# Kernel optimization log

Measured on AMD Instinct MI355X. Metric: run time of the kernel, lower is better.

Reference implementation:

```python
import jax, jax.numpy as jnp
import numpy as np

DIM = 1024
EPS = 1e-5


def setup_inputs() -> dict:
    key = jax.random.key(0)
    ks = jax.random.split(key, 7)
    C = DIM
    x = jax.random.normal(ks[0], (4, 4096, C), dtype=jnp.float32)
    norm_w = jnp.ones((C,), dtype=jnp.float32)
    norm_b = jnp.zeros((C,), dtype=jnp.float32)
    s = 1.0 / np.sqrt(C)
    qkv_w = jax.random.uniform(ks[1], (3 * C, C), dtype=jnp.float32, minval=-s, maxval=s)
    qkv_b = jax.random.uniform(ks[2], (3 * C,), dtype=jnp.float32, minval=-s, maxval=s)
    proj_w = jax.random.uniform(ks[3], (C, C), dtype=jnp.float32, minval=-s, maxval=s)
    proj_b = jax.random.uniform(ks[4], (C,), dtype=jnp.float32, minval=-s, maxval=s)
    return {"x": x, "norm_w": norm_w, "norm_b": norm_b, "qkv_w": qkv_w,
            "qkv_b": qkv_b, "proj_w": proj_w, "proj_b": proj_b}


def _layernorm(x, w, b):
    mu = jnp.mean(x, axis=-1, keepdims=True)
    var = jnp.mean(jnp.square(x - mu), axis=-1, keepdims=True)
    return (x - mu) * jax.lax.rsqrt(var + EPS) * w + b


def reference(x, norm_w, norm_b, qkv_w, qkv_b, proj_w, proj_b):
    B, T, C = x.shape
    residual = x
    h = _layernorm(x, norm_w, norm_b)
    qkv = jnp.einsum('btc,oc->bto', h, qkv_w) + qkv_b  # [B,T,3C]
    q, k, v = qkv[..., :C], qkv[..., C:2 * C], qkv[..., 2 * C:]
    attn = jnp.einsum('btc,bsc->bts', q, k) / jnp.sqrt(jnp.float32(C))  # raw QK^T, no softmax
    o = jnp.einsum('bts,bsc->btc', attn, v)
    o = jnp.einsum('btc,oc->bto', o, proj_w) + proj_b
    return residual + o  # dropout is identity in eval mode
```

## Files before the change

kernel.cpp:

```cpp
#include <hip/hip_runtime.h>

typedef _Float16 f16;
typedef _Float16 f16x4 __attribute__((ext_vector_type(4)));
typedef _Float16 f16x8 __attribute__((ext_vector_type(8)));
typedef float f32x4 __attribute__((ext_vector_type(4)));

#define AS1 __attribute__((address_space(1)))
#define AS3 __attribute__((address_space(3)))

__device__ __forceinline__ void gl_lds16(const f16* g, f16* l) {
  __builtin_amdgcn_global_load_lds((const AS1 void*)g, (AS3 void*)l, 16, 0, 0);
}

__global__ __launch_bounds__(256) void ln_kernel(const float* __restrict__ x,
                                                 const float* __restrict__ gw,
                                                 const float* __restrict__ gb,
                                                 f16* __restrict__ H) {
  const int wv = threadIdx.x >> 6, lane = threadIdx.x & 63;
  const long row = (long)blockIdx.x * 4 + wv;
  const float* xr = x + row * 1024;
  float4 v[4];
  float s = 0.f, s2 = 0.f;
#pragma unroll
  for (int j = 0; j < 4; ++j) {
    v[j] = ((const float4*)xr)[lane + 64 * j];
    s  += v[j].x + v[j].y + v[j].z + v[j].w;
    s2 += v[j].x * v[j].x + v[j].y * v[j].y + v[j].z * v[j].z + v[j].w * v[j].w;
  }
#pragma unroll
  for (int off = 32; off > 0; off >>= 1) {
    s  += __shfl_xor(s, off);
    s2 += __shfl_xor(s2, off);
  }
  const float mu = s * (1.0f / 1024.0f);
  const float rstd = rsqrtf(s2 * (1.0f / 1024.0f) - mu * mu + 1e-5f);
#pragma unroll
  for (int j = 0; j < 4; ++j) {
    const float4 w4 = ((const float4*)gw)[lane + 64 * j];
    const float4 b4 = ((const float4*)gb)[lane + 64 * j];
    f16x4 h;
    h[0] = (f16)((v[j].x - mu) * rstd * w4.x + b4.x);
    h[1] = (f16)((v[j].y - mu) * rstd * w4.y + b4.y);
    h[2] = (f16)((v[j].z - mu) * rstd * w4.z + b4.z);
    h[3] = (f16)((v[j].w - mu) * rstd * w4.w + b4.w);
    *(f16x4*)(H + row * 1024 + (lane + 64 * j) * 4) = h;
  }
}

__global__ __launch_bounds__(256) void transpose_cs_kernel(const f16* __restrict__ H,
                                                           f16* __restrict__ Ht,
                                                           float* __restrict__ hs) {
  __shared__ f16 tile[64][68];
  __shared__ float csum[4][64];
  const int b = blockIdx.z;
  const long Hb  = (long)b * 4096 * 1024;
  const long Htb = (long)b * 1024 * 4096;
  const int t0 = blockIdx.y * 64, c0 = blockIdx.x * 64;
  const int tid = threadIdx.x;
  const int r = tid >> 2, g0 = tid & 3;
#pragma unroll
  for (int i = 0; i < 4; ++i) {
    const int g = g0 + i * 4;
    f16x4 v = *(const f16x4*)(H + Hb + (long)(t0 + r) * 1024 + c0 + g * 4);
    *(f16x4*)&tile[r][g * 4] = v;
  }
  __syncthreads();
  {
    const int cl = tid & 63, rg = tid >> 6;
    float s = 0.f;
#pragma unroll
    for (int rr = 0; rr < 16; ++rr) s += (float)tile[rg * 16 + rr][cl];
    csum[rg][cl] = s;
  }
#pragma unroll
  for (int i = 0; i < 4; ++i) {
    const int g = g0 + i * 4;
    f16x4 v;
    v[0] = tile[g * 4 + 0][r];
    v[1] = tile[g * 4 + 1][r];
    v[2] = tile[g * 4 + 2][r];
    v[3] = tile[g * 4 + 3][r];
    *(f16x4*)(Ht + Htb + (long)(c0 + r) * 4096 + t0 + g * 4) = v;
  }
  __syncthreads();
  if (tid < 64)
    atomicAdd(&hs[b * 1024 + c0 + tid],
              csum[0][tid] + csum[1][tid] + csum[2][tid] + csum[3][tid]);
}

__global__ __launch_bounds__(256) void transcast4(const float* __restrict__ qkv_w,
                                                  const float* __restrict__ proj_w,
                                                  f16* __restrict__ WT3,
                                                  f16* __restrict__ Wh,
                                                  f16* __restrict__ Ph) {
  const int z = blockIdx.z;
  __shared__ f16 tile[64][68];
  const int r0 = blockIdx.y * 64, c0 = blockIdx.x * 64;
  const int tid = threadIdx.x;
  const int r = tid >> 2, g0 = tid & 3;
  if (z == 3) {
#pragma unroll
    for (int i = 0; i < 4; ++i) {
      const int g = g0 + i * 4;
      float4 v = *(const float4*)(proj_w + (long)(r0 + r) * 1024 + c0 + g * 4);
      f16x4 h; h[0]=(f16)v.x; h[1]=(f16)v.y; h[2]=(f16)v.z; h[3]=(f16)v.w;
      *(f16x4*)(Ph + (long)(r0 + r) * 1024 + c0 + g * 4) = h;
    }
    return;
  }
  const float* W = qkv_w + (long)z * 1048576;
  f16* WT = WT3 + (long)z * 1048576;
#pragma unroll
  for (int i = 0; i < 4; ++i) {
    const int g = g0 + i * 4;
    float4 v = *(const float4*)(W + (long)(r0 + r) * 1024 + c0 + g * 4);
    f16x4 h; h[0]=(f16)v.x; h[1]=(f16)v.y; h[2]=(f16)v.z; h[3]=(f16)v.w;
    *(f16x4*)&tile[r][g * 4] = h;
    if (z >= 1)
      *(f16x4*)(Wh + (long)z * 1048576 + (long)(r0 + r) * 1024 + c0 + g * 4) = h;
  }
  __syncthreads();
#pragma unroll
  for (int i = 0; i < 4; ++i) {
    const int g = g0 + i * 4;
    f16x4 v;
    v[0] = tile[g * 4 + 0][r];
    v[1] = tile[g * 4 + 1][r];
    v[2] = tile[g * 4 + 2][r];
    v[3] = tile[g * 4 + 3][r];
    *(f16x4*)(WT + (long)(c0 + r) * 1024 + r0 + g * 4) = v;
  }
}

__device__ __forceinline__ float dot1024(const f16* __restrict__ row,
                                         const float* __restrict__ v) {
  const int lane = threadIdx.x & 63;
  float s = 0.f;
#pragma unroll
  for (int j = 0; j < 2; ++j) {
    const int d = (lane + 64 * j) * 8;
    f16x8 a = *(const f16x8*)(row + d);
    float4 h0 = *(const float4*)(v + d);
    float4 h1 = *(const float4*)(v + d + 4);
    s += (float)a[0] * h0.x + (float)a[1] * h0.y + (float)a[2] * h0.z + (float)a[3] * h0.w
       + (float)a[4] * h1.x + (float)a[5] * h1.y + (float)a[6] * h1.z + (float)a[7] * h1.w;
  }
#pragma unroll
  for (int off = 32; off > 0; off >>= 1) s += __shfl_down(s, off);
  return s;
}

__device__ __forceinline__ float dotf1024(const float* __restrict__ a,
                                          const float* __restrict__ v) {
  const int lane = threadIdx.x & 63;
  float s = 0.f;
#pragma unroll
  for (int j = 0; j < 4; ++j) {
    const int d = (lane + 64 * j) * 4;
    float4 x = *(const float4*)(a + d);
    float4 q = *(const float4*)(v + d);
    s += x.x * q.x + x.y * q.y + x.z * q.z + x.w * q.w;
  }
#pragma unroll
  for (int off = 32; off > 0; off >>= 1) s += __shfl_down(s, off);
  return s;
}

__global__ void gemv3a(const f16* __restrict__ WT3, const f16* __restrict__ Ph,
                       const float* __restrict__ qkv_b, float* __restrict__ ayd,
                       float* __restrict__ scal) {
  if (blockIdx.x == 3072) {
    float s = dotf1024(qkv_b + 1024, qkv_b);
    if ((threadIdx.x & 63) == 0) scal[4] = s;
    return;
  }
  const int which = blockIdx.x >> 10, m = blockIdx.x & 1023;
  const f16* row;
  const float* v;
  if (which == 0)      { row = WT3 + (long)m * 1024;            v = qkv_b + 1024; }
  else if (which == 1) { row = WT3 + 1048576 + (long)m * 1024;  v = qkv_b; }
  else                 { row = Ph + (long)m * 1024;             v = qkv_b + 2048; }
  float s = dot1024(row, v);
  if ((threadIdx.x & 63) == 0) ayd[which * 1024 + m] = s;
}

__global__ void gemv3b(const f16* __restrict__ U, const f16* __restrict__ PWv,
                       const f16* __restrict__ Gh, const float* __restrict__ hs,
                       const float* __restrict__ ayd, float* __restrict__ efz,
                       float* __restrict__ scal) {
  if (blockIdx.x >= 12288) {
    const int b = blockIdx.x - 12288;
    float s = dotf1024(hs + b * 1024, ayd + 1024);
    if ((threadIdx.x & 63) == 0) scal[b] = s;
    return;
  }
  const int sel = blockIdx.x >> 12, r = blockIdx.x & 4095;
  const int b = r >> 10, m = r & 1023;
  const f16* row;
  const float* v;
  if (sel == 0)      { row = U + (long)m * 1024;                       v = hs + b * 1024; }
  else if (sel == 1) { row = PWv + (long)m * 1024;                     v = hs + b * 1024; }
  else               { row = Gh + (long)b * 1048576 + (long)m * 1024;  v = ayd + 1024; }
  float s = dot1024(row, v);
  if ((threadIdx.x & 63) == 0) efz[sel * 4096 + r] = s;
}

__global__ void gemvC2n(const f16* __restrict__ PWv, const float* __restrict__ efz,
                        const float* __restrict__ ayd, const float* __restrict__ scal,
                        const float* __restrict__ proj_b, float* __restrict__ c2) {
  const int b = blockIdx.x >> 10, c = blockIdx.x & 1023;
  float s = dot1024(PWv + (long)c * 1024, efz + 8192 + b * 1024);
  if ((threadIdx.x & 63) == 0) {
    const float d = ayd[2048 + c];
    c2[b * 1024 + c] = (s + d * scal[b] + scal[4] * (efz[4096 + b * 1024 + c] + 4096.f * d))
                         * 0.03125f + proj_b[c];
  }
}

#define GP64_COMMON()                                        \
  const int tid = threadIdx.x;                               \
  const int wave = tid >> 6, lane = tid & 63;                \
  const int lr = lane & 15, lk = lane >> 4;                  \
  const int srow = tid >> 3;                                 \
  const int slc  = (tid & 7) ^ (srow & 7);                   \
  const int kc0 = ((lk) ^ (lr & 7)) * 8;                     \
  const int kc1 = ((4 + lk) ^ (lr & 7)) * 8;

#define GEMM_WAIT8(NBUF_, r_)                                               \
  do {                                                                      \
    if constexpr (NBUF_ == 3) {                                             \
      if ((r_) >= 2)      asm volatile("s_waitcnt vmcnt(16)" ::: "memory"); \
      else if ((r_) == 1) asm volatile("s_waitcnt vmcnt(8)" ::: "memory");  \
      else                asm volatile("s_waitcnt vmcnt(0)" ::: "memory");  \
    } else {                                                                \
      if ((r_) >= 1)      asm volatile("s_waitcnt vmcnt(8)" ::: "memory");  \
      else                asm volatile("s_waitcnt vmcnt(0)" ::: "memory");  \
    }                                                                       \
  } while (0)

#define COMP64_HALF(asb_, bsb_, kc_)                                             \
  do {                                                                           \
    const f16* asb = (asb_);                                                     \
    const f16* bsb = (bsb_);                                                     \
    f16x8 af[4], bf[4];                                                          \
    _Pragma("unroll")                                                            \
    for (int mi = 0; mi < 4; ++mi)                                               \
      af[mi] = *(const f16x8*)(asb + (wm * 64 + mi * 16 + lr) * 64 + (kc_));     \
    _Pragma("unroll")                                                            \
    for (int ni = 0; ni < 4; ++ni)                                               \
      bf[ni] = *(const f16x8*)(bsb + (wn * 64 + ni * 16 + lr) * 64 + (kc_));     \
    _Pragma("unroll")                                                            \
    for (int mi = 0; mi < 4; ++mi)                                               \
      _Pragma("unroll")                                                          \
      for (int ni = 0; ni < 4; ++ni)                                             \
        acc[mi][ni] = __builtin_amdgcn_mfma_f32_16x16x32_f16(af[mi], bf[ni],     \
                                                             acc[mi][ni], 0, 0, 0); \
  } while (0)

#define GEMM_BODY_LOOP(NBUF_, NT_, STAGEM)                       \
  do {                                                           \
    if constexpr (NBUF_ == 3) {                                  \
      STAGEM(0, 0); STAGEM(1, 1);                                \
      int cur = 0, stg = 2;                                      \
      for (int t = 0; t < (NT_); ++t) {                          \
        if (t + 2 < (NT_)) STAGEM(stg, t + 2);                   \
        GEMM_WAIT8(3, (NT_) - 1 - t);                            \
        asm volatile("s_barrier" ::: "memory");                  \
        __builtin_amdgcn_s_setprio(1);                           \
        COMP64_HALF(&As[cur][0], &Bs[cur][0], kc0);              \
        COMP64_HALF(&As[cur][0], &Bs[cur][0], kc1);              \
        __builtin_amdgcn_s_setprio(0);                           \
        asm volatile("s_waitcnt lgkmcnt(0)" ::: "memory");       \
        asm volatile("s_barrier" ::: "memory");                  \
        cur = (cur + 1 == 3) ? 0 : cur + 1;                      \
        stg = (stg + 1 == 3) ? 0 : stg + 1;                      \
      }                                                          \
    } else {                                                     \
      STAGEM(0, 0);                                              \
      int cur = 0;                                               \
      for (int t = 0; t < (NT_); ++t) {                          \
        if (t + 1 < (NT_)) STAGEM(cur ^ 1, t + 1);               \
        GEMM_WAIT8(2, (NT_) - 1 - t);                            \
        asm volatile("s_barrier" ::: "memory");                  \
        __builtin_amdgcn_s_setprio(1);                           \
        COMP64_HALF(&As[cur][0], &Bs[cur][0], kc0);              \
        COMP64_HALF(&As[cur][0], &Bs[cur][0], kc1);              \
        __builtin_amdgcn_s_setprio(0);                           \
        asm volatile("s_waitcnt lgkmcnt(0)" ::: "memory");       \
        asm volatile("s_barrier" ::: "memory");                  \
        cur ^= 1;                                                \
      }                                                          \
    }                                                            \
  } while (0)

template <int MODE>
__global__ __launch_bounds__(256) void gemm128(
    const f16* __restrict__ A, const f16* __restrict__ B, int K,
    long sA, long sB, long sC,
    f16* __restrict__ Ch,
    const float* __restrict__ dvec, const float* __restrict__ evec,
    const float* __restrict__ fvec, const float* __restrict__ avec) {
  const int b = blockIdx.z;
  A += (long)b * sA;
  B += (long)b * sB;
  const int nx = blockIdx.y & 7;
  const int ny = blockIdx.x;

  GP64_COMMON();
  const int wm = wave >> 1, wn = wave & 1;

  __shared__ __align__(16) f16 As[3][8192];
  __shared__ __align__(16) f16 Bs[3][8192];

  const long aoffs = (long)(ny * 128 + srow) * K + slc * 8;
  const long boffs = (long)(nx * 128 + srow) * K + slc * 8;

  f32x4 zero = {0.f, 0.f, 0.f, 0.f};
  f32x4 acc[4][4];
#pragma unroll
  for (int mi = 0; mi < 4; ++mi)
#pragma unroll
    for (int ni = 0; ni < 4; ++ni) acc[mi][ni] = zero;

#define STAGE(buf, kt)                                                              \
  do {                                                                              \
    f16* asb = &As[buf][0];                                                         \
    f16* bsb = &Bs[buf][0];                                                         \
    _Pragma("unroll")                                                               \
    for (int q = 0; q < 4; ++q) {                                                   \
      gl_lds16(A + aoffs + (long)q * 32 * K + (kt) * 64, asb + q * 2048 + tid * 8); \
      gl_lds16(B + boffs + (long)q * 32 * K + (kt) * 64, bsb + q * 2048 + tid * 8); \
    }                                                                               \
  } while (0)

  const int nt = K >> 6;
  GEMM_BODY_LOOP(3, nt, STAGE);
#undef STAGE

  const long cb = (long)b * sC;
  const int m0 = ny * 128 + wm * 64;
  const int n0 = nx * 128 + wn * 64;
#pragma unroll
  for (int mi = 0; mi < 4; ++mi)
#pragma unroll
    for (int ni = 0; ni < 4; ++ni)
#pragma unroll
      for (int j = 0; j < 4; ++j) {
        const int gm = m0 + mi * 16 + lk * 4 + j;
        const int gn = n0 + ni * 16 + lr;
        float val = acc[mi][ni][j];
        if constexpr (MODE == 0) {
          Ch[cb + (long)gm * 1024 + gn] = (f16)val;
        } else {
          const float dm = dvec[gm];
          const float fm = fvec[b * 1024 + gm];
          const float en = evec[b * 1024 + gn];
          const float an = avec[gn];
          val = (val + dm * en + (fm + 4096.f * dm) * an) * 0.03125f;
          Ch[cb + (long)gm * 1024 + gn] = (f16)val;
        }
      }
}

__global__ __launch_bounds__(256) void gemmGUV(const f16* __restrict__ Ht,
                                               const f16* __restrict__ WT3,
                                               const f16* __restrict__ Ph,
                                               f16* __restrict__ part,
                                               f16* __restrict__ U,
                                               f16* __restrict__ PWv) {
  GP64_COMMON();
  const int wm = wave >> 1, wn = wave & 1;

  __shared__ __align__(16) f16 As[2][8192];
  __shared__ __align__(16) f16 Bs[2][8192];

  const int bid = blockIdx.x;
  const f16 *Ab, *Bb;
  long rs;
  int tileid = 0, zz = 0, selt = 0;
  if (bid < 576) {
    zz = bid & 15;
    tileid = bid >> 4;
    const int b = zz & 3, ks4 = zz >> 2;
    int ti = 0, trem = tileid;
    while (trem >= 8 - ti) { trem -= 8 - ti; ++ti; }
    const int tj = ti + trem;
    const f16* Hb = Ht + (long)b * 4194304;
    rs = 4096;
    Ab = Hb + (long)(ti * 128 + srow) * 4096 + (long)ks4 * 1024 + slc * 8;
    Bb = Hb + (long)(tj * 128 + srow) * 4096 + (long)ks4 * 1024 + slc * 8;
  } else {
    const int u = bid - 576;
    selt = (u >> 6) + 1;
    const int t = u & 63;
    const int ny = t >> 3, nxx = t & 7;
    const f16* A0 = (selt == 2) ? Ph : WT3;
    const f16* B0 = (selt == 2) ? (WT3 + 2097152) : (WT3 + 1048576);
    rs = 1024;
    Ab = A0 + (long)(ny * 128 + srow) * 1024 + slc * 8;
    Bb = B0 + (long)(nxx * 128 + srow) * 1024 + slc * 8;
  }

  f32x4 zero = {0.f, 0.f, 0.f, 0.f};
  f32x4 acc[4][4];
#pragma unroll
  for (int mi = 0; mi < 4; ++mi)
#pragma unroll
    for (int ni = 0; ni < 4; ++ni) acc[mi][ni] = zero;

#define STAGE(buf, kt)                                                            \
  do {                                                                            \
    f16* asb = &As[buf][0];                                                       \
    f16* bsb = &Bs[buf][0];                                                       \
    _Pragma("unroll")                                                             \
    for (int q = 0; q < 4; ++q) {                                                 \
      gl_lds16(Ab + (long)q * 32 * rs + (kt) * 64, asb + q * 2048 + tid * 8);     \
      gl_lds16(Bb + (long)q * 32 * rs + (kt) * 64, bsb + q * 2048 + tid * 8);     \
    }                                                                             \
  } while (0)

  GEMM_BODY_LOOP(2, 16, STAGE);
#undef STAGE

  if (selt == 0) {
    f16* P = part + ((long)zz * 36 + tileid) * 16384;
#pragma unroll
    for (int mi = 0; mi < 4; ++mi)
#pragma unroll
      for (int ni = 0; ni < 4; ++ni)
#pragma unroll
        for (int j = 0; j < 4; ++j) {
          const int gm = wm * 64 + mi * 16 + lk * 4 + j;
          const int gn = wn * 64 + ni * 16 + lr;
          P[gm * 128 + gn] = (f16)acc[mi][ni][j];
        }
  } else {
    const int u = bid - 576;
    const int t = u & 63;
    const int ny = t >> 3, nxx = t & 7;
    f16* C = (selt == 2) ? PWv : U;
    const int m0 = ny * 128 + wm * 64;
    const int n0 = nxx * 128 + wn * 64;
#pragma unroll
    for (int mi = 0; mi < 4; ++mi)
#pragma unroll
      for (int ni = 0; ni < 4; ++ni)
#pragma unroll
        for (int j = 0; j < 4; ++j) {
          const int gm = m0 + mi * 16 + lk * 4 + j;
          const int gn = n0 + ni * 16 + lr;
          C[(long)gm * 1024 + gn] = (f16)acc[mi][ni][j];
        }
  }
}

__global__ __launch_bounds__(512) void gemm256f(
    const f16* __restrict__ A,
    const f16* __restrict__ Bw,
    const float* __restrict__ resid,
    const float* __restrict__ c2v,
    float* __restrict__ outF) {
  const int lin = blockIdx.y * 4 + blockIdx.x;
  const int xcd = lin & 7, slot = lin >> 3;
  const int ny = xcd * 8 + (slot >> 2);
  const int nx = slot & 3;
  const int bb = ny >> 4;

  GP64_COMMON();
  const int wm = wave >> 2, wn = wave & 3;

  __shared__ __align__(16) f16 As[2][16384];
  __shared__ __align__(16) f16 Bs[2][16384];

  const f16* Ab = A + (long)ny * 262144;
  const f16* Bb = Bw + (long)bb * 1048576 + (long)nx * 262144;
  const long offs = (long)srow * 1024 + slc * 8;

  f32x4 zero = {0.f, 0.f, 0.f, 0.f};
  f32x4 acc[8][4];
#pragma unroll
  for (int mi = 0; mi < 8; ++mi)
#pragma unroll
    for (int ni = 0; ni < 4; ++ni) acc[mi][ni] = zero;

#define SA(buf, kt, q) gl_lds16(Ab + offs + (long)(q) * 65536 + (kt) * 64, &As[buf][(q) * 4096] + tid * 8)
#define SB(buf, kt, q) gl_lds16(Bb + offs + (long)(q) * 65536 + (kt) * 64, &Bs[buf][(q) * 4096] + tid * 8)

#define RD_BF(dst, bsb, kc)                                                       \
  _Pragma("unroll")                                                               \
  for (int ni = 0; ni < 4; ++ni)                                                  \
    dst[ni] = *(const f16x8*)((bsb) + (wn * 64 + ni * 16 + lr) * 64 + (kc));
#define RD_AF(dst, asb, mh, kc)                                                   \
  _Pragma("unroll")                                                               \
  for (int mi = 0; mi < 4; ++mi)                                                  \
    dst[mi] = *(const f16x8*)((asb) + (wm * 128 + (mh) * 64 + mi * 16 + lr) * 64 + (kc));
#define MF16(af_, bf_, mo)                                                        \
  __builtin_amdgcn_s_setprio(1);                                                  \
  _Pragma("unroll")                                                               \
  for (int mi = 0; mi < 4; ++mi)                                                  \
    _Pragma("unroll")                                                             \
    for (int ni = 0; ni < 4; ++ni)                                                \
      acc[(mo) + mi][ni] = __builtin_amdgcn_mfma_f32_16x16x32_f16(af_[mi], bf_[ni], \
                                                                  acc[(mo) + mi][ni], 0, 0, 0); \
  __builtin_amdgcn_s_setprio(0);

  const int nt = 16;
  SB(0, 0, 0); SB(0, 0, 1); SB(0, 0, 2); SB(0, 0, 3);
  SA(0, 0, 0); SA(0, 0, 2); SA(0, 0, 1); SA(0, 0, 3);

  int cur = 0;
  for (int t = 0; t < nt; ++t) {
    const f16* asb = &As[cur][0];
    const f16* bsb = &Bs[cur][0];
    const int nb = cur ^ 1;
    const bool st = (t + 1 < nt);
    f16x8 bf[4], af[4];

    asm volatile("s_waitcnt vmcnt(2)" ::: "memory");
    asm volatile("s_barrier" ::: "memory");
    RD_BF(bf, bsb, kc0);
    RD_AF(af, asb, 0, kc0);
    if (st) { SB(nb, t + 1, 0); SB(nb, t + 1, 1); }
    asm volatile("s_waitcnt lgkmcnt(0)" ::: "memory");
    MF16(af, bf, 0);
    asm volatile("s_barrier" ::: "memory");

    if (st) asm volatile("s_waitcnt vmcnt(2)" ::: "memory");
    else    asm volatile("s_waitcnt vmcnt(0)" ::: "memory");
    asm volatile("s_barrier" ::: "memory");
    RD_AF(af, asb, 1, kc0);
    if (st) { SB(nb, t + 1, 2); SB(nb, t + 1, 3); }
    asm volatile("s_waitcnt lgkmcnt(0)" ::: "memory");
    MF16(af, bf, 4);
    asm volatile("s_barrier" ::: "memory");

    RD_BF(bf, bsb, kc1);
    RD_AF(af, asb, 0, kc1);
    if (st) { SA(nb, t + 1, 0); SA(nb, t + 1, 2); }
    asm volatile("s_waitcnt lgkmcnt(0)" ::: "memory");
    MF16(af, bf, 0);
    asm volatile("s_barrier" ::: "memory");

    RD_AF(af, asb, 1, kc1);
    if (st) { SA(nb, t + 1, 1); SA(nb, t + 1, 3); }
    asm volatile("s_waitcnt lgkmcnt(0)" ::: "memory");
    MF16(af, bf, 4);
    asm volatile("s_barrier" ::: "memory");

    cur ^= 1;
  }
#undef SA
#undef SB
#undef RD_BF
#undef RD_AF
#undef MF16

  asm volatile("s_waitcnt vmcnt(0)" ::: "memory");
  asm volatile("s_barrier" ::: "memory");

  float* weps = ((float*)&As[0][0]) + wave * 1088;
  const int m0 = ny * 256 + wm * 128;
  const int n0 = nx * 256 + wn * 64;
  const int err = lane >> 3;
  const int ecc = (lane & 7) * 4;
  float4 cc2[2];
#pragma unroll
  for (int q = 0; q < 2; ++q)
    cc2[q] = *(const float4*)&c2v[bb * 1024 + n0 + ecc + 32 * q];

#pragma unroll
  for (int mi = 0; mi < 8; ++mi) {
#pragma unroll
    for (int ni = 0; ni < 4; ++ni)
#pragma unroll
      for (int j = 0; j < 4; ++j)
        weps[(lk * 4 + j) * 68 + ni * 16 + lr] = acc[mi][ni][j];
    asm volatile("s_waitcnt lgkmcnt(0)" ::: "memory");
#pragma unroll
    for (int h = 0; h < 2; ++h)
#pragma unroll
      for (int q = 0; q < 2; ++q) {
        const int rr = err + 8 * h;
        const int cc = ecc + 32 * q;
        float4 o = *(const float4*)&weps[rr * 68 + cc];
        const long gbase = (long)(m0 + mi * 16 + rr) * 1024 + n0 + cc;
        const float4 rv = *(const float4*)&resid[gbase];
        float4 ov;
        ov.x = o.x + rv.x + cc2[q].x;
        ov.y = o.y + rv.y + cc2[q].y;
        ov.z = o.z + rv.z + cc2[q].z;
        ov.w = o.w + rv.w + cc2[q].w;
        *(float4*)&outF[gbase] = ov;
      }
  }
}

__global__ __launch_bounds__(256) void treduce(const f16* __restrict__ part,
                                               f16* __restrict__ Gh) {
  const int tileid = blockIdx.x, b = blockIdx.y;
  int ti = 0, trem = tileid;
  while (trem >= 8 - ti) { trem -= 8 - ti; ++ti; }
  const int tj = ti + trem;
  __shared__ f16 tl[128][132];
  const int tid = threadIdx.x;
  f16* Gb = Gh + (long)b * 1048576;
#pragma unroll
  for (int it = 0; it < 16; ++it) {
    const int e = it * 1024 + tid * 4;
    const int r = e >> 7, c = e & 127;
    f16x4 p0 = *(const f16x4*)(part + ((long)(0 * 4 + b) * 36 + tileid) * 16384 + e);
    f16x4 p1 = *(const f16x4*)(part + ((long)(1 * 4 + b) * 36 + tileid) * 16384 + e);
    f16x4 p2 = *(const f16x4*)(part + ((long)(2 * 4 + b) * 36 + tileid) * 16384 + e);
    f16x4 p3 = *(const f16x4*)(part + ((long)(3 * 4 + b) * 36 + tileid) * 16384 + e);
    f16x4 sv;
#pragma unroll
    for (int j = 0; j < 4; ++j)
      sv[j] = (f16)((float)p0[j] + (float)p1[j] + (float)p2[j] + (float)p3[j]);
    *(f16x4*)(Gb + (long)(ti * 128 + r) * 1024 + tj * 128 + c) = sv;
    *(f16x4*)&tl[r][c] = sv;
  }
  if (ti != tj) {
    __syncthreads();
#pragma unroll
    for (int it = 0; it < 16; ++it) {
      const int e = it * 1024 + tid * 4;
      const int r = e >> 7, c = e & 127;
      f16x4 v;
      v[0] = tl[c + 0][r];
      v[1] = tl[c + 1][r];
      v[2] = tl[c + 2][r];
      v[3] = tl[c + 3][r];
      *(f16x4*)(Gb + (long)(tj * 128 + r) * 1024 + ti * 128 + c) = v;
    }
  }
}

extern "C" void kernel_launch(void* const* d_in, const int* in_sizes, int n_in,
                              void* d_out, int out_size, void* d_ws, size_t ws_size,
                              hipStream_t stream) {
  const float* x      = (const float*)d_in[0];
  const float* norm_w = (const float*)d_in[1];
  const float* norm_b = (const float*)d_in[2];
  const float* qkv_w  = (const float*)d_in[3];
  const float* qkv_b  = (const float*)d_in[4];
  const float* proj_w = (const float*)d_in[5];
  const float* proj_b = (const float*)d_in[6];
  float* out = (float*)d_out;
  char* ws = (char*)d_ws;

  const size_t OFF_H    = 0;
  const size_t OFF_HT   = 33554432;
  const size_t OFF_T1   = 33554432;
  const size_t OFF_T2   = 41943040;
  const size_t OFF_WH   = 67108864;
  const size_t OFF_PH   = 73400320;
  const size_t OFF_WT3  = 75497472;
  const size_t OFF_U    = 81788928;
  const size_t OFF_PWV  = 83886080;
  const size_t OFF_GH   = 85983232;
  const size_t OFF_PART = 94371840;
  const size_t OFF_HS   = 115343360;
  const size_t OFF_AYD  = 115392512;
  const size_t OFF_SCAL = 115404800;
  const size_t OFF_EFZ  = 115405824;
  const size_t OFF_C2   = 115471360;

  f16* H    = (f16*)(ws + OFF_H);
  f16* Ht   = (f16*)(ws + OFF_HT);
  f16* T1   = (f16*)(ws + OFF_T1);
  f16* T2   = (f16*)(ws + OFF_T2);
  f16* Wh   = (f16*)(ws + OFF_WH);
  f16* Ph   = (f16*)(ws + OFF_PH);
  f16* WT3  = (f16*)(ws + OFF_WT3);
  f16* U    = (f16*)(ws + OFF_U);
  f16* PWv  = (f16*)(ws + OFF_PWV);
  f16* Gh   = (f16*)(ws + OFF_GH);
  f16* part = (f16*)(ws + OFF_PART);
  float* hs   = (float*)(ws + OFF_HS);
  float* ayd  = (float*)(ws + OFF_AYD);
  float* scal = (float*)(ws + OFF_SCAL);
  float* efz  = (float*)(ws + OFF_EFZ);
  float* c2v  = (float*)(ws + OFF_C2);

  transcast4<<<dim3(16, 16, 4), 256, 0, stream>>>(qkv_w, proj_w, WT3, Wh, Ph);
  gemv3a<<<dim3(3073), 64, 0, stream>>>(WT3, Ph, qkv_b, ayd, scal);

  ln_kernel<<<dim3(4096), 256, 0, stream>>>(x, norm_w, norm_b, H);
  hipMemsetAsync(ws + OFF_HS, 0, 16384, stream);
  transpose_cs_kernel<<<dim3(16, 64, 4), 256, 0, stream>>>(H, Ht, hs);

  gemmGUV<<<dim3(704), 256, 0, stream>>>(Ht, WT3, Ph, part, U, PWv);
  treduce<<<dim3(36, 4), 256, 0, stream>>>(part, Gh);

  gemv3b<<<dim3(12292), 64, 0, stream>>>(U, PWv, Gh, hs, ayd, efz, scal);
  gemvC2n<<<dim3(4096), 64, 0, stream>>>(PWv, efz, ayd, scal, proj_b, c2v);

  gemm128<0><<<dim3(8, 8, 4), 256, 0, stream>>>(U, Gh, 1024, 0L, 1048576L, 1048576L,
      T1, nullptr, nullptr, nullptr, nullptr);
  gemm128<1><<<dim3(8, 8, 4), 256, 0, stream>>>(PWv, T1, 1024, 0L, 1048576L, 1048576L,
      T2, ayd + 2048, efz, efz + 4096, ayd);

  gemm256f<<<dim3(4, 64), 512, 0, stream>>>(H, T2, x, c2v, out);
}
```

Baseline: 195.8 us.

## Hand-schedule GEMM main loop with split A-tile prefetch and waitcnt control

Replaces the generic GEMM_BODY_LOOP in the fused GEMM kernel with a hand-written double-buffered loop. Each k-step is split into two halves, and the next tile's global-to-LDS loads are interleaved between them using explicit vmcnt/lgkmcnt waits and barriers. MFMA blocks are wrapped in s_setprio raises. The goal is to overlap memory loads with MFMA work more finely, at the cost of extra barriers and a fragile dependence on vmcnt counts matching the issue order.

```diff
diff --git a/kernel.cpp b/kernel.cpp
--- a/kernel.cpp
+++ b/kernel.cpp
@@ -408,19 +408,74 @@
 #pragma unroll
     for (int ni = 0; ni < 4; ++ni) acc[mi][ni] = zero;
 
-#define STAGE(buf, kt)                                                            \
-  do {                                                                            \
-    f16* asb = &As[buf][0];                                                       \
-    f16* bsb = &Bs[buf][0];                                                       \
-    _Pragma("unroll")                                                             \
-    for (int q = 0; q < 4; ++q) {                                                 \
-      gl_lds16(Ab + (long)q * 32 * rs + (kt) * 64, asb + q * 2048 + tid * 8);     \
-      gl_lds16(Bb + (long)q * 32 * rs + (kt) * 64, bsb + q * 2048 + tid * 8);     \
-    }                                                                             \
-  } while (0)
-
-  GEMM_BODY_LOOP(2, 16, STAGE);
-#undef STAGE
+#define SAq(buf, kt, q) gl_lds16(Ab + (long)(q) * 32 * rs + (kt) * 64, &As[buf][(q) * 2048] + tid * 8)
+#define SBq(buf, kt, q) gl_lds16(Bb + (long)(q) * 32 * rs + (kt) * 64, &Bs[buf][(q) * 2048] + tid * 8)
+
+  const int nt = 16;
+  SBq(0, 0, 0); SBq(0, 0, 1); SBq(0, 0, 2); SBq(0, 0, 3);
+  SAq(0, 0, 0); SAq(0, 0, 2); SAq(0, 0, 1); SAq(0, 0, 3);
+
+  int cur = 0;
+  for (int t = 0; t < nt; ++t) {
+    const f16* asb = &As[cur][0];
+    const f16* bsb = &Bs[cur][0];
+    const int nb = cur ^ 1;
+    const bool st = (t + 1 < nt);
+    f16x8 bf[4][2], af[2][2];
+
+    asm volatile("s_waitcnt vmcnt(2)" ::: "memory");
+    asm volatile("s_barrier" ::: "memory");
+#pragma unroll
+    for (int ni = 0; ni < 4; ++ni) {
+      bf[ni][0] = *(const f16x8*)(bsb + (wn * 64 + ni * 16 + lr) * 64 + kc0);
+      bf[ni][1] = *(const f16x8*)(bsb + (wn * 64 + ni * 16 + lr) * 64 + kc1);
+    }
+#pragma unroll
+    for (int mi = 0; mi < 2; ++mi) {
+      af[mi][0] = *(const f16x8*)(asb + (wm * 64 + mi * 16 + lr) * 64 + kc0);
+      af[mi][1] = *(const f16x8*)(asb + (wm * 64 + mi * 16 + lr) * 64 + kc1);
+    }
+    if (st) { SBq(nb, t + 1, 0); SBq(nb, t + 1, 1); SBq(nb, t + 1, 2); SBq(nb, t + 1, 3);
+              SAq(nb, t + 1, 0); SAq(nb, t + 1, 2); }
+    asm volatile("s_waitcnt lgkmcnt(0)" ::: "memory");
+    __builtin_amdgcn_s_setprio(1);
+#pragma unroll
+    for (int ks = 0; ks < 2; ++ks)
+#pragma unroll
+      for (int mi = 0; mi < 2; ++mi)
+#pragma unroll
+        for (int ni = 0; ni < 4; ++ni)
+          acc[mi][ni] = __builtin_amdgcn_mfma_f32_16x16x32_f16(af[mi][ks], bf[ni][ks],
+                                                               acc[mi][ni], 0, 0, 0);
+    __builtin_amdgcn_s_setprio(0);
+    asm volatile("s_barrier" ::: "memory");
+
+    if (st) asm volatile("s_waitcnt vmcnt(6)" ::: "memory");
+    else    asm volatile("s_waitcnt vmcnt(0)" ::: "memory");
+    asm volatile("s_barrier" ::: "memory");
+#pragma unroll
+    for (int mi = 0; mi < 2; ++mi) {
+      af[mi][0] = *(const f16x8*)(asb + (wm * 64 + (mi + 2) * 16 + lr) * 64 + kc0);
+      af[mi][1] = *(const f16x8*)(asb + (wm * 64 + (mi + 2) * 16 + lr) * 64 + kc1);
+    }
+    if (st) { SAq(nb, t + 1, 1); SAq(nb, t + 1, 3); }
+    asm volatile("s_waitcnt lgkmcnt(0)" ::: "memory");
+    __builtin_amdgcn_s_setprio(1);
+#pragma unroll
+    for (int ks = 0; ks < 2; ++ks)
+#pragma unroll
+      for (int mi = 0; mi < 2; ++mi)
+#pragma unroll
+        for (int ni = 0; ni < 4; ++ni)
+          acc[mi + 2][ni] = __builtin_amdgcn_mfma_f32_16x16x32_f16(af[mi][ks], bf[ni][ks],
+                                                                   acc[mi + 2][ni], 0, 0, 0);
+    __builtin_amdgcn_s_setprio(0);
+    asm volatile("s_barrier" ::: "memory");
+
+    cur ^= 1;
+  }
+#undef SAq
+#undef SBq
 
   if (selt == 0) {
     f16* P = part + ((long)zz * 36 + tileid) * 16384;
```

Measured after the change: 190.0 us. 2.9% less time.

## Fuse GEMV passes into batched GEMMs and use finer-grained pipelined main loop

Applied to the files above, without the earlier changes.

The standalone gemv3b and gemvC2n launches are merged into the two batched T1/T2 GEMM launches as extra blocks, with four waves per block each doing one dot product. The hs memset moves into the layernorm kernel. All three GEMMs switch to a new double-buffered loop that issues next-tile loads in quarters, interleaved between two half-tile MFMA phases. This cuts launch count and aims to overlap GEMV work with GEMM tiles, at the cost of more barriers and more complex wait counts.

```diff
diff --git a/kernel.cpp b/kernel.cpp
--- a/kernel.cpp
+++ b/kernel.cpp
@@ -15,7 +15,13 @@
 __global__ __launch_bounds__(256) void ln_kernel(const float* __restrict__ x,
                                                  const float* __restrict__ gw,
                                                  const float* __restrict__ gb,
-                                                 f16* __restrict__ H) {
+                                                 f16* __restrict__ H,
+                                                 float* __restrict__ hs) {
+  if (blockIdx.x == 0) {
+#pragma unroll
+    for (int j = 0; j < 4; ++j)
+      ((float4*)hs)[threadIdx.x + 256 * j] = make_float4(0.f, 0.f, 0.f, 0.f);
+  }
   const int wv = threadIdx.x >> 6, lane = threadIdx.x & 63;
   const long row = (long)blockIdx.x * 4 + wv;
   const float* xr = x + row * 1024;
@@ -184,39 +190,6 @@
   if ((threadIdx.x & 63) == 0) ayd[which * 1024 + m] = s;
 }
 
-__global__ void gemv3b(const f16* __restrict__ U, const f16* __restrict__ PWv,
-                       const f16* __restrict__ Gh, const float* __restrict__ hs,
-                       const float* __restrict__ ayd, float* __restrict__ efz,
-                       float* __restrict__ scal) {
-  if (blockIdx.x >= 12288) {
-    const int b = blockIdx.x - 12288;
-    float s = dotf1024(hs + b * 1024, ayd + 1024);
-    if ((threadIdx.x & 63) == 0) scal[b] = s;
-    return;
-  }
-  const int sel = blockIdx.x >> 12, r = blockIdx.x & 4095;
-  const int b = r >> 10, m = r & 1023;
-  const f16* row;
-  const float* v;
-  if (sel == 0)      { row = U + (long)m * 1024;                       v = hs + b * 1024; }
-  else if (sel == 1) { row = PWv + (long)m * 1024;                     v = hs + b * 1024; }
-  else               { row = Gh + (long)b * 1048576 + (long)m * 1024;  v = ayd + 1024; }
-  float s = dot1024(row, v);
-  if ((threadIdx.x & 63) == 0) efz[sel * 4096 + r] = s;
-}
-
-__global__ void gemvC2n(const f16* __restrict__ PWv, const float* __restrict__ efz,
-                        const float* __restrict__ ayd, const float* __restrict__ scal,
-                        const float* __restrict__ proj_b, float* __restrict__ c2) {
-  const int b = blockIdx.x >> 10, c = blockIdx.x & 1023;
-  float s = dot1024(PWv + (long)c * 1024, efz + 8192 + b * 1024);
-  if ((threadIdx.x & 63) == 0) {
-    const float d = ayd[2048 + c];
-    c2[b * 1024 + c] = (s + d * scal[b] + scal[4] * (efz[4096 + b * 1024 + c] + 4096.f * d))
-                         * 0.03125f + proj_b[c];
-  }
-}
-
 #define GP64_COMMON()                                        \
   const int tid = threadIdx.x;                               \
   const int wave = tid >> 6, lane = tid & 63;                \
@@ -226,94 +199,100 @@
   const int kc0 = ((lk) ^ (lr & 7)) * 8;                     \
   const int kc1 = ((4 + lk) ^ (lr & 7)) * 8;
 
-#define GEMM_WAIT8(NBUF_, r_)                                               \
-  do {                                                                      \
-    if constexpr (NBUF_ == 3) {                                             \
-      if ((r_) >= 2)      asm volatile("s_waitcnt vmcnt(16)" ::: "memory"); \
-      else if ((r_) == 1) asm volatile("s_waitcnt vmcnt(8)" ::: "memory");  \
-      else                asm volatile("s_waitcnt vmcnt(0)" ::: "memory");  \
-    } else {                                                                \
-      if ((r_) >= 1)      asm volatile("s_waitcnt vmcnt(8)" ::: "memory");  \
-      else                asm volatile("s_waitcnt vmcnt(0)" ::: "memory");  \
-    }                                                                       \
-  } while (0)
-
-#define COMP64_HALF(asb_, bsb_, kc_)                                             \
-  do {                                                                           \
-    const f16* asb = (asb_);                                                     \
-    const f16* bsb = (bsb_);                                                     \
-    f16x8 af[4], bf[4];                                                          \
-    _Pragma("unroll")                                                            \
-    for (int mi = 0; mi < 4; ++mi)                                               \
-      af[mi] = *(const f16x8*)(asb + (wm * 64 + mi * 16 + lr) * 64 + (kc_));     \
-    _Pragma("unroll")                                                            \
-    for (int ni = 0; ni < 4; ++ni)                                               \
-      bf[ni] = *(const f16x8*)(bsb + (wn * 64 + ni * 16 + lr) * 64 + (kc_));     \
-    _Pragma("unroll")                                                            \
-    for (int mi = 0; mi < 4; ++mi)                                               \
-      _Pragma("unroll")                                                          \
-      for (int ni = 0; ni < 4; ++ni)                                             \
-        acc[mi][ni] = __builtin_amdgcn_mfma_f32_16x16x32_f16(af[mi], bf[ni],     \
-                                                             acc[mi][ni], 0, 0, 0); \
-  } while (0)
-
-#define GEMM_BODY_LOOP(NBUF_, NT_, STAGEM)                       \
-  do {                                                           \
-    if constexpr (NBUF_ == 3) {                                  \
-      STAGEM(0, 0); STAGEM(1, 1);                                \
-      int cur = 0, stg = 2;                                      \
-      for (int t = 0; t < (NT_); ++t) {                          \
-        if (t + 2 < (NT_)) STAGEM(stg, t + 2);                   \
-        GEMM_WAIT8(3, (NT_) - 1 - t);                            \
-        asm volatile("s_barrier" ::: "memory");                  \
-        __builtin_amdgcn_s_setprio(1);                           \
-        COMP64_HALF(&As[cur][0], &Bs[cur][0], kc0);              \
-        COMP64_HALF(&As[cur][0], &Bs[cur][0], kc1);              \
-        __builtin_amdgcn_s_setprio(0);                           \
-        asm volatile("s_waitcnt lgkmcnt(0)" ::: "memory");       \
-        asm volatile("s_barrier" ::: "memory");                  \
-        cur = (cur + 1 == 3) ? 0 : cur + 1;                      \
-        stg = (stg + 1 == 3) ? 0 : stg + 1;                      \
-      }                                                          \
-    } else {                                                     \
-      STAGEM(0, 0);                                              \
-      int cur = 0;                                               \
-      for (int t = 0; t < (NT_); ++t) {                          \
-        if (t + 1 < (NT_)) STAGEM(cur ^ 1, t + 1);               \
-        GEMM_WAIT8(2, (NT_) - 1 - t);                            \
-        asm volatile("s_barrier" ::: "memory");                  \
-        __builtin_amdgcn_s_setprio(1);                           \
-        COMP64_HALF(&As[cur][0], &Bs[cur][0], kc0);              \
-        COMP64_HALF(&As[cur][0], &Bs[cur][0], kc1);              \
-        __builtin_amdgcn_s_setprio(0);                           \
-        asm volatile("s_waitcnt lgkmcnt(0)" ::: "memory");       \
-        asm volatile("s_barrier" ::: "memory");                  \
-        cur ^= 1;                                                \
-      }                                                          \
-    }                                                            \
-  } while (0)
-
-template <int MODE>
-__global__ __launch_bounds__(256) void gemm128(
-    const f16* __restrict__ A, const f16* __restrict__ B, int K,
-    long sA, long sB, long sC,
-    f16* __restrict__ Ch,
-    const float* __restrict__ dvec, const float* __restrict__ evec,
-    const float* __restrict__ fvec, const float* __restrict__ avec) {
-  const int b = blockIdx.z;
-  A += (long)b * sA;
-  B += (long)b * sB;
-  const int nx = blockIdx.y & 7;
-  const int ny = blockIdx.x;
-
+#define FINE2_LOOP(NT_)                                                            \
+  SBq(0, 0, 0); SBq(0, 0, 1); SBq(0, 0, 2); SBq(0, 0, 3);                          \
+  SAq(0, 0, 0); SAq(0, 0, 2); SAq(0, 0, 1); SAq(0, 0, 3);                          \
+  int cur = 0;                                                                     \
+  for (int t = 0; t < (NT_); ++t) {                                                \
+    const f16* asb = &As[cur][0];                                                  \
+    const f16* bsb = &Bs[cur][0];                                                  \
+    const int nb = cur ^ 1;                                                        \
+    const bool st = (t + 1 < (NT_));                                               \
+    f16x8 bf[4][2], af[2][2];                                                      \
+    asm volatile("s_waitcnt vmcnt(2)" ::: "memory");                               \
+    asm volatile("s_barrier" ::: "memory");                                        \
+    _Pragma("unroll")                                                              \
+    for (int ni = 0; ni < 4; ++ni) {                                               \
+      bf[ni][0] = *(const f16x8*)(bsb + (wn * 64 + ni * 16 + lr) * 64 + kc0);      \
+      bf[ni][1] = *(const f16x8*)(bsb + (wn * 64 + ni * 16 + lr) * 64 + kc1);      \
+    }                                                                              \
+    _Pragma("unroll")                                                              \
+    for (int mi = 0; mi < 2; ++mi) {                                               \
+      af[mi][0] = *(const f16x8*)(asb + (wm * 64 + mi * 16 + lr) * 64 + kc0);      \
+      af[mi][1] = *(const f16x8*)(asb + (wm * 64 + mi * 16 + lr) * 64 + kc1);      \
+    }                                                                              \
+    if (st) { SBq(nb, t + 1, 0); SBq(nb, t + 1, 1); SBq(nb, t + 1, 2);             \
+              SBq(nb, t + 1, 3); SAq(nb, t + 1, 0); SAq(nb, t + 1, 2); }           \
+    asm volatile("s_waitcnt lgkmcnt(0)" ::: "memory");                             \
+    __builtin_amdgcn_s_setprio(1);                                                 \
+    _Pragma("unroll")                                                              \
+    for (int ks = 0; ks < 2; ++ks)                                                 \
+      _Pragma("unroll")                                                            \
+      for (int mi = 0; mi < 2; ++mi)                                               \
+        _Pragma("unroll")                                                          \
+        for (int ni = 0; ni < 4; ++ni)                                             \
+          acc[mi][ni] = __builtin_amdgcn_mfma_f32_16x16x32_f16(af[mi][ks],         \
+                            bf[ni][ks], acc[mi][ni], 0, 0, 0);                     \
+    __builtin_amdgcn_s_setprio(0);                                                 \
+    asm volatile("s_barrier" ::: "memory");                                        \
+    if (st) asm volatile("s_waitcnt vmcnt(6)" ::: "memory");                       \
+    else    asm volatile("s_waitcnt vmcnt(0)" ::: "memory");                       \
+    asm volatile("s_barrier" ::: "memory");                                        \
+    _Pragma("unroll")                                                              \
+    for (int mi = 0; mi < 2; ++mi) {                                               \
+      af[mi][0] = *(const f16x8*)(asb + (wm * 64 + (mi + 2) * 16 + lr) * 64 + kc0);\
+      af[mi][1] = *(const f16x8*)(asb + (wm * 64 + (mi + 2) * 16 + lr) * 64 + kc1);\
+    }                                                                              \
+    if (st) { SAq(nb, t + 1, 1); SAq(nb, t + 1, 3); }                              \
+    asm volatile("s_waitcnt lgkmcnt(0)" ::: "memory");                             \
+    __builtin_amdgcn_s_setprio(1);                                                 \
+    _Pragma("unroll")                                                              \
+    for (int ks = 0; ks < 2; ++ks)                                                 \
+      _Pragma("unroll")                                                            \
+      for (int mi = 0; mi < 2; ++mi)                                               \
+        _Pragma("unroll")                                                          \
+        for (int ni = 0; ni < 4; ++ni)                                             \
+          acc[mi + 2][ni] = __builtin_amdgcn_mfma_f32_16x16x32_f16(af[mi][ks],     \
+                                bf[ni][ks], acc[mi + 2][ni], 0, 0, 0);             \
+    __builtin_amdgcn_s_setprio(0);                                                 \
+    asm volatile("s_barrier" ::: "memory");                                        \
+    cur ^= 1;                                                                      \
+  }
+
+__global__ __launch_bounds__(256) void gemmT1_g3b(
+    const f16* __restrict__ U, const f16* __restrict__ Gh, f16* __restrict__ T1,
+    const f16* __restrict__ PWv, const float* __restrict__ hs,
+    const float* __restrict__ ayd, float* __restrict__ efz,
+    float* __restrict__ scal) {
   GP64_COMMON();
+  __shared__ __align__(16) f16 As[2][8192];
+  __shared__ __align__(16) f16 Bs[2][8192];
+
+  const int bid = blockIdx.x;
+  if (bid >= 256) {
+    const int u = (bid - 256) * 4 + wave;
+    if (u >= 12288) {
+      const int b = u - 12288;
+      float s = dotf1024(hs + b * 1024, ayd + 1024);
+      if (lane == 0) scal[b] = s;
+      return;
+    }
+    const int sel = u >> 12, r = u & 4095;
+    const int b = r >> 10, m = r & 1023;
+    const f16* row;
+    const float* v;
+    if (sel == 0)      { row = U + (long)m * 1024;                       v = hs + b * 1024; }
+    else if (sel == 1) { row = PWv + (long)m * 1024;                     v = hs + b * 1024; }
+    else               { row = Gh + (long)b * 1048576 + (long)m * 1024;  v = ayd + 1024; }
+    float s = dot1024(row, v);
+    if (lane == 0) efz[sel * 4096 + r] = s;
+    return;
+  }
+
+  const int ny = bid & 7, nx = (bid >> 3) & 7, b = bid >> 6;
   const int wm = wave >> 1, wn = wave & 1;
-
-  __shared__ __align__(16) f16 As[3][8192];
-  __shared__ __align__(16) f16 Bs[3][8192];
-
-  const long aoffs = (long)(ny * 128 + srow) * K + slc * 8;
-  const long boffs = (long)(nx * 128 + srow) * K + slc * 8;
+  const f16* Ab = U + (long)(ny * 128 + srow) * 1024 + slc * 8;
+  const f16* Bb = Gh + (long)b * 1048576 + (long)(nx * 128 + srow) * 1024 + slc * 8;
 
   f32x4 zero = {0.f, 0.f, 0.f, 0.f};
   f32x4 acc[4][4];
@@ -322,22 +301,13 @@
 #pragma unroll
     for (int ni = 0; ni < 4; ++ni) acc[mi][ni] = zero;
 
-#define STAGE(buf, kt)                                                              \
-  do {                                                                              \
-    f16* asb = &As[buf][0];                                                         \
-    f16* bsb = &Bs[buf][0];                                                         \
-    _Pragma("unroll")                                                               \
-    for (int q = 0; q < 4; ++q) {                                                   \
-      gl_lds16(A + aoffs + (long)q * 32 * K + (kt) * 64, asb + q * 2048 + tid * 8); \
-      gl_lds16(B + boffs + (long)q * 32 * K + (kt) * 64, bsb + q * 2048 + tid * 8); \
-    }                                                                               \
-  } while (0)
-
-  const int nt = K >> 6;
-  GEMM_BODY_LOOP(3, nt, STAGE);
-#undef STAGE
-
-  const long cb = (long)b * sC;
+#define SAq(buf, kt, q) gl_lds16(Ab + (long)(q) * 32768 + (kt) * 64, &As[buf][(q) * 2048] + tid * 8)
+#define SBq(buf, kt, q) gl_lds16(Bb + (long)(q) * 32768 + (kt) * 64, &Bs[buf][(q) * 2048] + tid * 8)
+  FINE2_LOOP(16)
+#undef SAq
+#undef SBq
+
+  f16* C = T1 + (long)b * 1048576;
   const int m0 = ny * 128 + wm * 64;
   const int n0 = nx * 128 + wn * 64;
 #pragma unroll
@@ -348,17 +318,67 @@
       for (int j = 0; j < 4; ++j) {
         const int gm = m0 + mi * 16 + lk * 4 + j;
         const int gn = n0 + ni * 16 + lr;
-        float val = acc[mi][ni][j];
-        if constexpr (MODE == 0) {
-          Ch[cb + (long)gm * 1024 + gn] = (f16)val;
-        } else {
-          const float dm = dvec[gm];
-          const float fm = fvec[b * 1024 + gm];
-          const float en = evec[b * 1024 + gn];
-          const float an = avec[gn];
-          val = (val + dm * en + (fm + 4096.f * dm) * an) * 0.03125f;
-          Ch[cb + (long)gm * 1024 + gn] = (f16)val;
-        }
+        C[(long)gm * 1024 + gn] = (f16)acc[mi][ni][j];
+      }
+}
+
+__global__ __launch_bounds__(256) void gemmW2_c2(
+    const f16* __restrict__ PWv, const f16* __restrict__ T1, f16* __restrict__ T2,
+    const float* __restrict__ ayd, const float* __restrict__ efz,
+    const float* __restrict__ scal, const float* __restrict__ proj_b,
+    float* __restrict__ c2v) {
+  GP64_COMMON();
+  __shared__ __align__(16) f16 As[2][8192];
+  __shared__ __align__(16) f16 Bs[2][8192];
+
+  const int bid = blockIdx.x;
+  if (bid >= 256) {
+    const int u = (bid - 256) * 4 + wave;
+    const int b = u >> 10, c = u & 1023;
+    float s = dot1024(PWv + (long)c * 1024, efz + 8192 + b * 1024);
+    if (lane == 0) {
+      const float d = ayd[2048 + c];
+      c2v[b * 1024 + c] = (s + d * scal[b] + scal[4] * (efz[4096 + b * 1024 + c] + 4096.f * d))
+                            * 0.03125f + proj_b[c];
+    }
+    return;
+  }
+
+  const int ny = bid & 7, nx = (bid >> 3) & 7, b = bid >> 6;
+  const int wm = wave >> 1, wn = wave & 1;
+  const f16* Ab = PWv + (long)(ny * 128 + srow) * 1024 + slc * 8;
+  const f16* Bb = T1 + (long)b * 1048576 + (long)(nx * 128 + srow) * 1024 + slc * 8;
+
+  f32x4 zero = {0.f, 0.f, 0.f, 0.f};
+  f32x4 acc[4][4];
+#pragma unroll
+  for (int mi = 0; mi < 4; ++mi)
+#pragma unroll
+    for (int ni = 0; ni < 4; ++ni) acc[mi][ni] = zero;
+
+#define SAq(buf, kt, q) gl_lds16(Ab + (long)(q) * 32768 + (kt) * 64, &As[buf][(q) * 2048] + tid * 8)
+#define SBq(buf, kt, q) gl_lds16(Bb + (long)(q) * 32768 + (kt) * 64, &Bs[buf][(q) * 2048] + tid * 8)
+  FINE2_LOOP(16)
+#undef SAq
+#undef SBq
+
+  f16* C = T2 + (long)b * 1048576;
+  const int m0 = ny * 128 + wm * 64;
+  const int n0 = nx * 128 + wn * 64;
+#pragma unroll
+  for (int mi = 0; mi < 4; ++mi)
+#pragma unroll
+    for (int ni = 0; ni < 4; ++ni)
+#pragma unroll
+      for (int j = 0; j < 4; ++j) {
+        const int gm = m0 + mi * 16 + lk * 4 + j;
+        const int gn = n0 + ni * 16 + lr;
+        const float dm = ayd[2048 + gm];
+        const float fm = efz[4096 + b * 1024 + gm];
+        const float en = efz[b * 1024 + gn];
+        const float an = ayd[gn];
+        float val = (acc[mi][ni][j] + dm * en + (fm + 4096.f * dm) * an) * 0.03125f;
+        C[(long)gm * 1024 + gn] = (f16)val;
       }
 }
 
@@ -408,19 +428,11 @@
 #pragma unroll
     for (int ni = 0; ni < 4; ++ni) acc[mi][ni] = zero;
 
-#define STAGE(buf, kt)                                                            \
-  do {                                                                            \
-    f16* asb = &As[buf][0];                                                       \
-    f16* bsb = &Bs[buf][0];                                                       \
-    _Pragma("unroll")                                                             \
-    for (int q = 0; q < 4; ++q) {                                                 \
-      gl_lds16(Ab + (long)q * 32 * rs + (kt) * 64, asb + q * 2048 + tid * 8);     \
-      gl_lds16(Bb + (long)q * 32 * rs + (kt) * 64, bsb + q * 2048 + tid * 8);     \
-    }                                                                             \
-  } while (0)
-
-  GEMM_BODY_LOOP(2, 16, STAGE);
-#undef STAGE
+#define SAq(buf, kt, q) gl_lds16(Ab + (long)(q) * 32 * rs + (kt) * 64, &As[buf][(q) * 2048] + tid * 8)
+#define SBq(buf, kt, q) gl_lds16(Bb + (long)(q) * 32 * rs + (kt) * 64, &Bs[buf][(q) * 2048] + tid * 8)
+  FINE2_LOOP(16)
+#undef SAq
+#undef SBq
 
   if (selt == 0) {
     f16* P = part + ((long)zz * 36 + tileid) * 16384;
@@ -685,20 +697,14 @@
   transcast4<<<dim3(16, 16, 4), 256, 0, stream>>>(qkv_w, proj_w, WT3, Wh, Ph);
   gemv3a<<<dim3(3073), 64, 0, stream>>>(WT3, Ph, qkv_b, ayd, scal);
 
-  ln_kernel<<<dim3(4096), 256, 0, stream>>>(x, norm_w, norm_b, H);
-  hipMemsetAsync(ws + OFF_HS, 0, 16384, stream);
+  ln_kernel<<<dim3(4096), 256, 0, stream>>>(x, norm_w, norm_b, H, hs);
   transpose_cs_kernel<<<dim3(16, 64, 4), 256, 0, stream>>>(H, Ht, hs);
 
   gemmGUV<<<dim3(704), 256, 0, stream>>>(Ht, WT3, Ph, part, U, PWv);
   treduce<<<dim3(36, 4), 256, 0, stream>>>(part, Gh);
 
-  gemv3b<<<dim3(12292), 64, 0, stream>>>(U, PWv, Gh, hs, ayd, efz, scal);
-  gemvC2n<<<dim3(4096), 64, 0, stream>>>(PWv, efz, ayd, scal, proj_b, c2v);
-
-  gemm128<0><<<dim3(8, 8, 4), 256, 0, stream>>>(U, Gh, 1024, 0L, 1048576L, 1048576L,
-      T1, nullptr, nullptr, nullptr, nullptr);
-  gemm128<1><<<dim3(8, 8, 4), 256, 0, stream>>>(PWv, T1, 1024, 0L, 1048576L, 1048576L,
-      T2, ayd + 2048, efz, efz + 4096, ayd);
+  gemmT1_g3b<<<dim3(3329), 256, 0, stream>>>(U, Gh, T1, PWv, hs, ayd, efz, scal);
+  gemmW2_c2<<<dim3(1280), 256, 0, stream>>>(PWv, T1, T2, ayd, efz, scal, proj_b, c2v);
 
   gemm256f<<<dim3(4, 64), 512, 0, stream>>>(H, T2, x, c2v, out);
 }
```

After: 178.5 us. -8.8%, faster.
